# Optimization experiments

Measured on AMD Instinct MI355X. Metric: run time of the kernel, lower is better.

## Reference

```python
import jax, jax.numpy as jnp
import numpy as np
import math

B, L, DIM, H = 2, 2048, 512, 8


def setup_inputs() -> dict:
    key = jax.random.key(0)
    ks = jax.random.split(key, 8)
    s = 0.02
    return {
        "x": jax.random.normal(ks[0], (B, L, DIM), dtype=jnp.float32),
        "Wq": jax.random.normal(ks[1], (DIM, DIM), dtype=jnp.float32) * s,
        "Wk": jax.random.normal(ks[2], (DIM, DIM), dtype=jnp.float32) * s,
        "Wv": jax.random.normal(ks[3], (DIM, DIM), dtype=jnp.float32) * s,
        "Wb": jax.random.normal(ks[4], (H, DIM), dtype=jnp.float32) * s,   # content_bias weight
        "mixing": jax.random.normal(ks[5], (H, DIM), dtype=jnp.float32) * 0.2,  # UNIFORM init, std=0.2
        "Wd": jax.random.normal(ks[6], (DIM, DIM), dtype=jnp.float32) * s,
        "bd": jax.random.normal(ks[7], (DIM,), dtype=jnp.float32) * s,
    }


def reference(x, Wq, Wk, Wv, Wb, mixing, Wd, bd):
    b, l, d = x.shape
    h = mixing.shape[0]
    dh = d // h
    q = x @ Wq.T                      # [B,L,D]
    k = x @ Wk.T                      # [B,S,D]
    v = (x @ Wv.T).reshape(b, l, h, dh).transpose(0, 2, 1, 3)  # [B,H,S,dh]
    # scores[b,h,l,s] = sum_d q[b,l,d] * mixing[h,d] * k[b,s,d]
    scores = jnp.einsum("bld,hd,bsd->bhls", q, mixing, k)
    # content bias: [B,S,H] -> broadcast over query positions as [B,H,1,S]
    cb = jnp.einsum("bsd,hd->bhs", x, Wb)
    scale = math.sqrt(d / h)  # attention_head_size = dim / num_heads
    scores = (scores + cb[:, :, None, :]) / scale
    probs = jax.nn.softmax(scores, axis=-1)   # dropout disabled (eval)
    ctx = jnp.einsum("bhls,bhsd->bhld", probs, v)  # [B,H,L,dh]
    ctx = ctx.transpose(0, 2, 1, 3).reshape(b, l, d)
    return ctx @ Wd.T + bd
```

## Files before the change

### kernel.cpp

```cpp
#include <hip/hip_runtime.h>

#define B_ 2
#define L_ 2048
#define D_ 512
#define H_ 8
#define S_ 2048

typedef __attribute__((ext_vector_type(8))) short short8;
typedef __attribute__((ext_vector_type(8))) unsigned short ushort8;
typedef __attribute__((ext_vector_type(4))) unsigned short ushort4v;
typedef __attribute__((ext_vector_type(4))) float f32x4;
typedef __attribute__((ext_vector_type(16))) float f32x16;
typedef __attribute__((ext_vector_type(4))) float float4v;

__device__ __forceinline__ unsigned short f2bf(float f) {
    unsigned u = __float_as_uint(f);
    u += 0x7FFF + ((u >> 16) & 1);
    return (unsigned short)(u >> 16);
}
__device__ __forceinline__ float bf2f(unsigned short s) {
    return __uint_as_float(((unsigned)s) << 16);
}
__device__ __forceinline__ int swap23(int x) {
    return (x & ~12) | ((x & 4) << 1) | ((x & 8) >> 1);
}
__device__ __forceinline__ void async16(void* lds, const void* g) {
    __builtin_amdgcn_global_load_lds(
        (const __attribute__((address_space(1))) void*)(g),
        (__attribute__((address_space(3))) void*)(lds), 16, 0, 0);
}

__global__ __launch_bounds__(256) void cvt_cb(const float* __restrict__ x,
                                              const float* __restrict__ w0, const float* __restrict__ w1,
                                              const float* __restrict__ w2, const float* __restrict__ w3,
                                              const float* __restrict__ Wb,
                                              unsigned short* __restrict__ xb,
                                              unsigned short* __restrict__ d0, unsigned short* __restrict__ d1,
                                              unsigned short* __restrict__ d2, unsigned short* __restrict__ d3,
                                              float* __restrict__ cb) {
    if (blockIdx.x < 3072) {
        int i = blockIdx.x * 256 + threadIdx.x;
        const float* s;
        unsigned short* d;
        int idx;
        if (i < 524288) { s = x; d = xb; idx = i; }
        else {
            int off = i - 524288;
            int wsel = off >> 16; idx = off & 65535;
            s = (wsel == 0) ? w0 : (wsel == 1) ? w1 : (wsel == 2) ? w2 : w3;
            d = (wsel == 0) ? d0 : (wsel == 1) ? d1 : (wsel == 2) ? d2 : d3;
        }
        float4v v = *(const float4v*)(s + (size_t)idx * 4);
        ushort4v o;
        o[0] = f2bf(v[0]); o[1] = f2bf(v[1]); o[2] = f2bf(v[2]); o[3] = f2bf(v[3]);
        *(ushort4v*)(d + (size_t)idx * 4) = o;
    } else {
        const int tid = threadIdx.x, w = tid >> 6, lane = tid & 63;
        const int row = (blockIdx.x - 3072) * 4 + w;
        const int h = lane >> 3, seg = lane & 7;
        const float* xp = x + (size_t)row * 512 + seg * 64;
        const float* wp = Wb + (size_t)h * 512 + seg * 64;
        float acc = 0.f;
        #pragma unroll
        for (int j = 0; j < 16; ++j) {
            float4v xv = *(const float4v*)(xp + j * 4);
            float4v wv = *(const float4v*)(wp + j * 4);
            acc += xv[0] * wv[0] + xv[1] * wv[1] + xv[2] * wv[2] + xv[3] * wv[3];
        }
        acc += __shfl_xor(acc, 1);
        acc += __shfl_xor(acc, 2);
        acc += __shfl_xor(acc, 4);
        if (seg == 0) {
            int b = row >> 11, s = row & 2047;
            cb[((size_t)(b * H_ + h)) * S_ + s] = acc * 0.125f;
        }
    }
}

__device__ __forceinline__ void gemm128_core(const unsigned short* __restrict__ Ap,
                                             const unsigned short* __restrict__ Bp,
                                             short* sA, short* sB, int tid, f32x4 c[4][4]) {
    const int w = tid >> 6, lane = tid & 63, quad = lane >> 4, l15 = lane & 15;
    const int wm = (w >> 1) * 64, wn = (w & 1) * 64;
    for (int kc = 0; kc < 8; ++kc) {
        __syncthreads();
        #pragma unroll
        for (int j = 0; j < 4; ++j) {
            int i = tid + j * 256;
            int row = i >> 3, seg = i & 7;
            *(ushort8*)&sA[row * 72 + seg * 8] = *(const ushort8*)(Ap + (size_t)row * 512 + kc * 64 + seg * 8);
            *(ushort8*)&sB[row * 72 + seg * 8] = *(const ushort8*)(Bp + (size_t)row * 512 + kc * 64 + seg * 8);
        }
        __syncthreads();
        #pragma unroll
        for (int ks = 0; ks < 2; ++ks) {
            short8 a[4], b[4];
            #pragma unroll
            for (int ii = 0; ii < 4; ++ii)
                a[ii] = *(const short8*)&sA[(wm + ii * 16 + l15) * 72 + ks * 32 + quad * 8];
            #pragma unroll
            for (int jj = 0; jj < 4; ++jj)
                b[jj] = *(const short8*)&sB[(wn + jj * 16 + l15) * 72 + ks * 32 + quad * 8];
            #pragma unroll
            for (int ii = 0; ii < 4; ++ii)
                #pragma unroll
                for (int jj = 0; jj < 4; ++jj)
                    c[ii][jj] = __builtin_amdgcn_mfma_f32_16x16x32_bf16(a[ii], b[jj], c[ii][jj], 0, 0, 0);
        }
    }
}

__global__ __launch_bounds__(256) void gemm_qkv(const unsigned short* __restrict__ xb,
                                                const unsigned short* __restrict__ Wqb,
                                                const unsigned short* __restrict__ Wkb,
                                                const unsigned short* __restrict__ Wvb,
                                                unsigned short* __restrict__ qb,
                                                unsigned short* __restrict__ kpack,
                                                unsigned short* __restrict__ vfrag) {
    __shared__ short sA[128 * 72];
    __shared__ short sB[128 * 72];
    const int m0 = blockIdx.x * 128, n0 = blockIdx.y * 128, z = blockIdx.z;
    const unsigned short* Bsel = (z == 0) ? Wqb : ((z == 1) ? Wkb : Wvb);
    f32x4 c[4][4];
    #pragma unroll
    for (int ii = 0; ii < 4; ++ii)
        #pragma unroll
        for (int jj = 0; jj < 4; ++jj) { f32x4 zv = {0.f, 0.f, 0.f, 0.f}; c[ii][jj] = zv; }
    gemm128_core(xb + (size_t)m0 * 512, Bsel + (size_t)n0 * 512, sA, sB, threadIdx.x, c);
    const int tid = threadIdx.x, w = tid >> 6, lane = tid & 63, quad = lane >> 4, l15 = lane & 15;
    const int wm = (w >> 1) * 64, wn = (w & 1) * 64;
    #pragma unroll
    for (int ii = 0; ii < 4; ++ii) {
        const int mb = m0 + wm + ii * 16 + quad * 4;
        const int bb = mb >> 11;
        if (z == 0) {
            #pragma unroll
            for (int jj = 0; jj < 4; ++jj) {
                int ncol = n0 + wn + jj * 16 + l15;
                #pragma unroll
                for (int r = 0; r < 4; ++r)
                    qb[(size_t)(mb + r) * 512 + ncol] = f2bf(c[ii][jj][r]);
            }
        } else if (z == 1) {
            #pragma unroll
            for (int jj = 0; jj < 4; ++jj) {
                int d = n0 + wn + jj * 16 + l15;
                int f = d >> 4, hid = (d >> 3) & 1, jq = d & 7;
                #pragma unroll
                for (int r = 0; r < 4; ++r) {
                    int s = (mb + r) & 2047;
                    int t = s >> 5, rr = swap23(s & 31);
                    kpack[(((size_t)(bb * 64 + t)) * 32 + f) * 512 + hid * 256 + rr * 8 + jq]
                        = f2bf(c[ii][jj][r]);
                }
            }
        } else {
            const int hh = (n0 + wn) >> 6;
            const int s = mb & 2047;
            #pragma unroll
            for (int jj = 0; jj < 4; ++jj) {
                int dh = jj * 16 + l15;
                ushort4v o;
                o[0] = f2bf(c[ii][jj][0]); o[1] = f2bf(c[ii][jj][1]);
                o[2] = f2bf(c[ii][jj][2]); o[3] = f2bf(c[ii][jj][3]);
                size_t blk = ((size_t)(bb * H_ + hh) * 64 + (s >> 5)) * 4
                           + ((dh >> 5) * 2 + ((s >> 4) & 1));
                *(ushort4v*)(vfrag + blk * 512 + (dh & 31) * 8 + ((s >> 3) & 1) * 256 + (s & 7)) = o;
            }
        }
    }
}

__global__ __launch_bounds__(256) void gemm_out(const unsigned short* __restrict__ ctxb,
                                                const unsigned short* __restrict__ Wdb,
                                                const float* __restrict__ bd,
                                                float* __restrict__ out) {
    __shared__ short sA[128 * 72];
    __shared__ short sB[128 * 72];
    const int m0 = blockIdx.x * 128, n0 = blockIdx.y * 128;
    f32x4 c[4][4];
    #pragma unroll
    for (int ii = 0; ii < 4; ++ii)
        #pragma unroll
        for (int jj = 0; jj < 4; ++jj) { f32x4 zv = {0.f, 0.f, 0.f, 0.f}; c[ii][jj] = zv; }
    gemm128_core(ctxb + (size_t)m0 * 512, Wdb + (size_t)n0 * 512, sA, sB, threadIdx.x, c);
    const int tid = threadIdx.x, w = tid >> 6, lane = tid & 63, quad = lane >> 4, l15 = lane & 15;
    const int wm = (w >> 1) * 64, wn = (w & 1) * 64;
    #pragma unroll
    for (int ii = 0; ii < 4; ++ii) {
        const int mb = m0 + wm + ii * 16 + quad * 4;
        #pragma unroll
        for (int jj = 0; jj < 4; ++jj) {
            int ncol = n0 + wn + jj * 16 + l15;
            float bias = bd[ncol];
            #pragma unroll
            for (int r = 0; r < 4; ++r)
                out[(size_t)(mb + r) * 512 + ncol] = c[ii][jj][r] + bias;
        }
    }
}

__global__ __launch_bounds__(256, 2) void flash_attn(const unsigned short* __restrict__ qb,
                                                     const unsigned short* __restrict__ kpack,
                                                     const unsigned short* __restrict__ vfrag,
                                                     const float* __restrict__ cb_all,
                                                     const float* __restrict__ mixing,
                                                     _Float16* __restrict__ Opart,
                                                     float* __restrict__ lpart) {
    __shared__ short sK[4][8192];
    const int bid = blockIdx.x;
    const int half = bid & 1, b = (bid >> 1) & 1, h = (bid >> 2) & 7, qt = bid >> 5;
    const int tid = threadIdx.x, w = tid >> 6, lane = tid & 63;
    const int l31 = lane & 31, hi = lane >> 5;
    const int q0 = qt * 128 + w * 32;
    const unsigned short* kbase = kpack + ((size_t)(b * 64 + half * 32)) * 32 * 512;
    const unsigned short* vfb = vfrag + ((size_t)(b * H_ + h) * 64 + half * 32) * 2048;
    const float* cbp = cb_all + (size_t)(b * H_ + h) * S_ + half * 1024;
    const float* mixh = mixing + h * D_;

    short8 qf[32];
    {
        const unsigned short* qrow = qb + ((size_t)(b * L_) + q0 + l31) * D_ + hi * 8;
        #pragma unroll
        for (int i = 0; i < 32; ++i) {
            ushort8 qv = *(const ushort8*)(qrow + i * 16);
            float4v ma = *(const float4v*)(mixh + i * 16 + hi * 8);
            float4v mb = *(const float4v*)(mixh + i * 16 + hi * 8 + 4);
            short8 ov;
            ov[0] = (short)f2bf(bf2f(qv[0]) * ma[0]);
            ov[1] = (short)f2bf(bf2f(qv[1]) * ma[1]);
            ov[2] = (short)f2bf(bf2f(qv[2]) * ma[2]);
            ov[3] = (short)f2bf(bf2f(qv[3]) * ma[3]);
            ov[4] = (short)f2bf(bf2f(qv[4]) * mb[0]);
            ov[5] = (short)f2bf(bf2f(qv[5]) * mb[1]);
            ov[6] = (short)f2bf(bf2f(qv[6]) * mb[2]);
            ov[7] = (short)f2bf(bf2f(qv[7]) * mb[3]);
            qf[i] = ov;
        }
    }
    asm volatile("s_waitcnt vmcnt(0)" ::: "memory");

    f32x16 acco0, acco1;
    #pragma unroll
    for (int i = 0; i < 16; ++i) { acco0[i] = 0.f; acco1[i] = 0.f; }
    float lsum = 0.f;
    f32x16 accsA, accsB;
    short8 av00, av01, av10, av11;

    auto stageK = [&](int p) {
        const char* src = (const char*)(kbase + (size_t)p * 8192);
        char* dst = (char*)&sK[p & 3][0];
        #pragma unroll
        for (int ii = 0; ii < 4; ++ii)
            async16(dst + w * 1024 + ii * 4096, src + w * 1024 + ii * 4096 + (size_t)lane * 16);
    };
    auto ldV = [&](int t) {
        const unsigned short* vp = vfb + (size_t)t * 2048 + lane * 8;
        av00 = *(const short8*)(vp);
        av01 = *(const short8*)(vp + 512);
        av10 = *(const short8*)(vp + 1024);
        av11 = *(const short8*)(vp + 1536);
        asm volatile("" ::: "memory");
    };
    auto qk_chunk = [&](const short* buf, int qbase) {
        __builtin_amdgcn_s_setprio(1);
        #pragma unroll
        for (int f = 0; f < 16; ++f) {
            short8 a = *(const short8*)&buf[f * 512 + lane * 8];
            if (f & 1) accsB = __builtin_amdgcn_mfma_f32_32x32x16_bf16(a, qf[qbase + f], accsB, 0, 0, 0);
            else       accsA = __builtin_amdgcn_mfma_f32_32x32x16_bf16(a, qf[qbase + f], accsA, 0, 0, 0);
        }
        __builtin_amdgcn_s_setprio(0);
    };
    auto softmax_pv = [&](int t) {
        const int s0 = t * 32;
        float p[16];
        #pragma unroll
        for (int R = 0; R < 16; ++R) {
            const int cr = (R & 3) + 8 * (R >> 2);
            const int idx = s0 + cr - 4 * ((R >> 2) & 1);
            float cbA = cbp[idx];
            float cbB = cbp[idx + 8];
            float cbv = hi ? cbB : cbA;
            float pe = __expf((accsA[R] + accsB[R]) * 0.125f + cbv);
            p[R] = pe;
            lsum += pe;
        }
        union { unsigned int u[4]; short8 s8; } P0, P1;
        #pragma unroll
        for (int j = 0; j < 4; ++j) {
            P0.u[j] = __builtin_amdgcn_perm(__float_as_uint(p[2 * j + 1]) + 0x8000u,
                                            __float_as_uint(p[2 * j]) + 0x8000u, 0x07060302u);
            P1.u[j] = __builtin_amdgcn_perm(__float_as_uint(p[8 + 2 * j + 1]) + 0x8000u,
                                            __float_as_uint(p[8 + 2 * j]) + 0x8000u, 0x07060302u);
        }
        __builtin_amdgcn_s_setprio(1);
        acco0 = __builtin_amdgcn_mfma_f32_32x32x16_bf16(av00, P0.s8, acco0, 0, 0, 0);
        acco0 = __builtin_amdgcn_mfma_f32_32x32x16_bf16(av01, P1.s8, acco0, 0, 0, 0);
        acco1 = __builtin_amdgcn_mfma_f32_32x32x16_bf16(av10, P0.s8, acco1, 0, 0, 0);
        acco1 = __builtin_amdgcn_mfma_f32_32x32x16_bf16(av11, P1.s8, acco1, 0, 0, 0);
        __builtin_amdgcn_s_setprio(0);
    };

    stageK(0); stageK(1); stageK(2);

    for (int t = 0; t < 31; ++t) {
        #pragma unroll
        for (int i = 0; i < 16; ++i) { accsA[i] = 0.f; accsB[i] = 0.f; }
        const short* be = &sK[(t & 1) << 1][0];
        const short* bo = &sK[((t & 1) << 1) | 1][0];
        asm volatile("s_waitcnt vmcnt(8)" ::: "memory");
        __builtin_amdgcn_s_barrier();
        ldV(t);
        stageK(2 * t + 3);
        qk_chunk(be, 0);
        asm volatile("s_waitcnt vmcnt(12)" ::: "memory");
        __builtin_amdgcn_s_barrier();
        if (t < 30) stageK(2 * t + 4);
        qk_chunk(bo, 16);
        asm volatile("s_waitcnt vmcnt(8)" ::: "memory");
        softmax_pv(t);
    }
    {
        #pragma unroll
        for (int i = 0; i < 16; ++i) { accsA[i] = 0.f; accsB[i] = 0.f; }
        asm volatile("s_waitcnt vmcnt(8)" ::: "memory");
        __builtin_amdgcn_s_barrier();
        ldV(31);
        qk_chunk(&sK[2][0], 0);
        asm volatile("s_waitcnt vmcnt(4)" ::: "memory");
        __builtin_amdgcn_s_barrier();
        qk_chunk(&sK[3][0], 16);
        asm volatile("s_waitcnt vmcnt(0)" ::: "memory");
        softmax_pv(31);
    }

    lsum += __shfl_xor(lsum, 32);
    if (hi == 0) lpart[(size_t)bid * 128 + w * 32 + l31] = lsum;
    #pragma unroll
    for (int R = 0; R < 16; ++R) {
        int dh = (R & 3) + 8 * (R >> 2) + 4 * hi;
        Opart[((size_t)bid * 64 + dh) * 128 + w * 32 + l31] = (_Float16)acco0[R];
        Opart[((size_t)bid * 64 + 32 + dh) * 128 + w * 32 + l31] = (_Float16)acco1[R];
    }
}

__global__ __launch_bounds__(256) void merge_ctx(const _Float16* __restrict__ Opart,
                                                 const float* __restrict__ lpart,
                                                 unsigned short* __restrict__ ctxb) {
    int t = blockIdx.x * 256 + threadIdx.x;
    int qq = t & 127, dh4 = (t >> 7) & 15, qt = (t >> 11) & 15, h = (t >> 15) & 7, b = t >> 18;
    int base = (qt << 5) | (h << 2) | (b << 1);
    float l = lpart[(size_t)base * 128 + qq] + lpart[(size_t)(base + 1) * 128 + qq];
    float inv = 1.f / l;
    ushort4v o;
    #pragma unroll
    for (int e = 0; e < 4; ++e) {
        int dh = dh4 * 4 + e;
        float v = (float)Opart[((size_t)base * 64 + dh) * 128 + qq]
                + (float)Opart[((size_t)(base + 1) * 64 + dh) * 128 + qq];
        o[e] = f2bf(v * inv);
    }
    *(ushort4v*)(ctxb + ((size_t)(b * L_) + qt * 128 + qq) * 512 + h * 64 + dh4 * 4) = o;
}

extern "C" void kernel_launch(void* const* d_in, const int* in_sizes, int n_in,
                              void* d_out, int out_size, void* d_ws, size_t ws_size,
                              hipStream_t stream) {
    (void)in_sizes; (void)n_in; (void)out_size; (void)ws_size;
    const float* x      = (const float*)d_in[0];
    const float* Wq     = (const float*)d_in[1];
    const float* Wk     = (const float*)d_in[2];
    const float* Wv     = (const float*)d_in[3];
    const float* Wb     = (const float*)d_in[4];
    const float* mixing = (const float*)d_in[5];
    const float* Wd     = (const float*)d_in[6];
    const float* bd     = (const float*)d_in[7];
    float* out = (float*)d_out;

    char* ws = (char*)d_ws;
    const size_t MiB = 1048576;
    unsigned short* xb    = (unsigned short*)(ws);
    unsigned short* qb    = (unsigned short*)(ws + 4 * MiB);
    unsigned short* kpack = (unsigned short*)(ws + 8 * MiB);
    unsigned short* vfrag = (unsigned short*)(ws + 12 * MiB);
    unsigned short* ctxb  = (unsigned short*)(ws + 16 * MiB);
    unsigned short* Wqb   = (unsigned short*)(ws + 20 * MiB);
    unsigned short* Wkb   = (unsigned short*)(ws + 20 * MiB + 512 * 1024);
    unsigned short* Wvb   = (unsigned short*)(ws + 21 * MiB);
    unsigned short* Wdb   = (unsigned short*)(ws + 21 * MiB + 512 * 1024);
    float* cbuf           = (float*)(ws + 22 * MiB);
    float* lpart          = (float*)(ws + 23 * MiB);
    _Float16* Opart       = (_Float16*)(ws + 24 * MiB);

    cvt_cb<<<4096, 256, 0, stream>>>(x, Wq, Wk, Wv, Wd, Wb, xb, Wqb, Wkb, Wvb, Wdb, cbuf);
    gemm_qkv<<<dim3(32, 4, 3), 256, 0, stream>>>(xb, Wqb, Wkb, Wvb, qb, kpack, vfrag);
    flash_attn<<<512, 256, 0, stream>>>(qb, kpack, vfrag, cbuf, mixing, Opart, lpart);
    merge_ctx<<<2048, 256, 0, stream>>>(Opart, lpart, ctxb);
    gemm_out<<<dim3(32, 4), 256, 0, stream>>>(ctxb, Wdb, bd, out);
}
```

Baseline: 217.6 us.

## Switch QK score MFMAs to FP8 with scaled K/Q and bf16 content bias

Measured after the change: 200.6 us. -7.8%, faster.

```diff
diff --git a/kernel.cpp b/kernel.cpp
--- a/kernel.cpp
+++ b/kernel.cpp
@@ -20,6 +20,18 @@
 }
 __device__ __forceinline__ float bf2f(unsigned short s) {
     return __uint_as_float(((unsigned)s) << 16);
+}
+__device__ __forceinline__ unsigned char f2fp8(float f) {
+    return (unsigned char)(__builtin_amdgcn_cvt_pk_fp8_f32(f, f, 0, false) & 0xff);
+}
+__device__ __forceinline__ long pack8fp8(const float* v) {
+    int lo = __builtin_amdgcn_cvt_pk_fp8_f32(v[0], v[1], 0, false);
+    lo = __builtin_amdgcn_cvt_pk_fp8_f32(v[2], v[3], lo, true);
+    int hi = __builtin_amdgcn_cvt_pk_fp8_f32(v[4], v[5], 0, false);
+    hi = __builtin_amdgcn_cvt_pk_fp8_f32(v[6], v[7], hi, true);
+    union { int i[2]; long l; } u;
+    u.i[0] = lo; u.i[1] = hi;
+    return u.l;
 }
 __device__ __forceinline__ int swap23(int x) {
     return (x & ~12) | ((x & 4) << 1) | ((x & 8) >> 1);
@@ -37,7 +49,7 @@
                                               unsigned short* __restrict__ xb,
                                               unsigned short* __restrict__ d0, unsigned short* __restrict__ d1,
                                               unsigned short* __restrict__ d2, unsigned short* __restrict__ d3,
-                                              float* __restrict__ cb) {
+                                              unsigned short* __restrict__ cb) {
     if (blockIdx.x < 3072) {
         int i = blockIdx.x * 256 + threadIdx.x;
         const float* s;
@@ -72,7 +84,7 @@
         acc += __shfl_xor(acc, 4);
         if (seg == 0) {
             int b = row >> 11, s = row & 2047;
-            cb[((size_t)(b * H_ + h)) * S_ + s] = acc * 0.125f;
+            cb[((size_t)(b * H_ + h)) * S_ + s] = f2bf(acc * 0.125f);
         }
     }
 }
@@ -115,7 +127,7 @@
                                                 const unsigned short* __restrict__ Wkb,
                                                 const unsigned short* __restrict__ Wvb,
                                                 unsigned short* __restrict__ qb,
-                                                unsigned short* __restrict__ kpack,
+                                                unsigned char* __restrict__ kpack8,
                                                 unsigned short* __restrict__ vfrag) {
     __shared__ short sA[128 * 72];
     __shared__ short sB[128 * 72];
@@ -145,13 +157,13 @@
             #pragma unroll
             for (int jj = 0; jj < 4; ++jj) {
                 int d = n0 + wn + jj * 16 + l15;
-                int f = d >> 4, hid = (d >> 3) & 1, jq = d & 7;
+                int pair = d >> 5, fh = (d >> 4) & 1, hid = (d >> 3) & 1, jq = d & 7;
                 #pragma unroll
                 for (int r = 0; r < 4; ++r) {
                     int s = (mb + r) & 2047;
                     int t = s >> 5, rr = swap23(s & 31);
-                    kpack[(((size_t)(bb * 64 + t)) * 32 + f) * 512 + hid * 256 + rr * 8 + jq]
-                        = f2bf(c[ii][jj][r]);
+                    kpack8[(((size_t)(bb * 64 + t) * 16 + pair) << 10)
+                           + (hid * 32 + rr) * 16 + fh * 8 + jq] = f2fp8(c[ii][jj][r] * 32.f);
                 }
             }
         } else {
@@ -201,24 +213,24 @@
 }
 
 __global__ __launch_bounds__(256, 2) void flash_attn(const unsigned short* __restrict__ qb,
-                                                     const unsigned short* __restrict__ kpack,
+                                                     const unsigned char* __restrict__ kpack8,
                                                      const unsigned short* __restrict__ vfrag,
-                                                     const float* __restrict__ cb_all,
+                                                     const unsigned short* __restrict__ cb_all,
                                                      const float* __restrict__ mixing,
                                                      _Float16* __restrict__ Opart,
                                                      float* __restrict__ lpart) {
-    __shared__ short sK[4][8192];
+    __shared__ char sK[4][8192];
     const int bid = blockIdx.x;
     const int half = bid & 1, b = (bid >> 1) & 1, h = (bid >> 2) & 7, qt = bid >> 5;
     const int tid = threadIdx.x, w = tid >> 6, lane = tid & 63;
     const int l31 = lane & 31, hi = lane >> 5;
     const int q0 = qt * 128 + w * 32;
-    const unsigned short* kbase = kpack + ((size_t)(b * 64 + half * 32)) * 32 * 512;
+    const unsigned char* kbase = kpack8 + (((size_t)(b * 64 + half * 32)) << 14);
     const unsigned short* vfb = vfrag + ((size_t)(b * H_ + h) * 64 + half * 32) * 2048;
-    const float* cbp = cb_all + (size_t)(b * H_ + h) * S_ + half * 1024;
+    const unsigned short* cbq = cb_all + (size_t)(b * H_ + h) * S_ + half * 1024;
     const float* mixh = mixing + h * D_;
 
-    short8 qf[32];
+    long qq[32];
     {
         const unsigned short* qrow = qb + ((size_t)(b * L_) + q0 + l31) * D_ + hi * 8;
         #pragma unroll
@@ -226,16 +238,16 @@
             ushort8 qv = *(const ushort8*)(qrow + i * 16);
             float4v ma = *(const float4v*)(mixh + i * 16 + hi * 8);
             float4v mb = *(const float4v*)(mixh + i * 16 + hi * 8 + 4);
-            short8 ov;
-            ov[0] = (short)f2bf(bf2f(qv[0]) * ma[0]);
-            ov[1] = (short)f2bf(bf2f(qv[1]) * ma[1]);
-            ov[2] = (short)f2bf(bf2f(qv[2]) * ma[2]);
-            ov[3] = (short)f2bf(bf2f(qv[3]) * ma[3]);
-            ov[4] = (short)f2bf(bf2f(qv[4]) * mb[0]);
-            ov[5] = (short)f2bf(bf2f(qv[5]) * mb[1]);
-            ov[6] = (short)f2bf(bf2f(qv[6]) * mb[2]);
-            ov[7] = (short)f2bf(bf2f(qv[7]) * mb[3]);
-            qf[i] = ov;
+            float v[8];
+            v[0] = bf2f(qv[0]) * ma[0] * 16.f;
+            v[1] = bf2f(qv[1]) * ma[1] * 16.f;
+            v[2] = bf2f(qv[2]) * ma[2] * 16.f;
+            v[3] = bf2f(qv[3]) * ma[3] * 16.f;
+            v[4] = bf2f(qv[4]) * mb[0] * 16.f;
+            v[5] = bf2f(qv[5]) * mb[1] * 16.f;
+            v[6] = bf2f(qv[6]) * mb[2] * 16.f;
+            v[7] = bf2f(qv[7]) * mb[3] * 16.f;
+            qq[i] = pack8fp8(v);
         }
     }
     asm volatile("s_waitcnt vmcnt(0)" ::: "memory");
@@ -246,12 +258,13 @@
     float lsum = 0.f;
     f32x16 accsA, accsB;
     short8 av00, av01, av10, av11;
+    ushort8 cbr0, cbr1, cbr2, cbr3;
 
     auto stageK = [&](int p) {
-        const char* src = (const char*)(kbase + (size_t)p * 8192);
-        char* dst = (char*)&sK[p & 3][0];
-        #pragma unroll
-        for (int ii = 0; ii < 4; ++ii)
+        const char* src = (const char*)kpack8 + (((size_t)(b * 64 + half * 32)) << 14) + (size_t)p * 8192;
+        char* dst = &sK[p & 3][0];
+        #pragma unroll
+        for (int ii = 0; ii < 2; ++ii)
             async16(dst + w * 1024 + ii * 4096, src + w * 1024 + ii * 4096 + (size_t)lane * 16);
     };
     auto ldV = [&](int t) {
@@ -262,27 +275,40 @@
         av11 = *(const short8*)(vp + 1536);
         asm volatile("" ::: "memory");
     };
-    auto qk_chunk = [&](const short* buf, int qbase) {
+    auto ldCB = [&](int t) {
+        const unsigned short* cp = cbq + t * 32;
+        cbr0 = *(const ushort8*)(cp);
+        cbr1 = *(const ushort8*)(cp + 8);
+        cbr2 = *(const ushort8*)(cp + 16);
+        cbr3 = *(const ushort8*)(cp + 24);
+        asm volatile("" ::: "memory");
+    };
+    auto qk_chunk = [&](const char* buf, int qbase) {
         __builtin_amdgcn_s_setprio(1);
         #pragma unroll
-        for (int f = 0; f < 16; ++f) {
-            short8 a = *(const short8*)&buf[f * 512 + lane * 8];
-            if (f & 1) accsB = __builtin_amdgcn_mfma_f32_32x32x16_bf16(a, qf[qbase + f], accsB, 0, 0, 0);
-            else       accsA = __builtin_amdgcn_mfma_f32_32x32x16_bf16(a, qf[qbase + f], accsA, 0, 0, 0);
+        for (int p = 0; p < 8; ++p) {
+            long a0, a1;
+            {
+                const long* ap = (const long*)&buf[p * 1024 + lane * 16];
+                a0 = ap[0];
+                a1 = ap[1];
+            }
+            accsA = __builtin_amdgcn_mfma_f32_32x32x16_fp8_fp8(a0, qq[qbase + 2 * p], accsA, 0, 0, 0);
+            accsB = __builtin_amdgcn_mfma_f32_32x32x16_fp8_fp8(a1, qq[qbase + 2 * p + 1], accsB, 0, 0, 0);
         }
         __builtin_amdgcn_s_setprio(0);
     };
-    auto softmax_pv = [&](int t) {
-        const int s0 = t * 32;
+    auto softmax_pv = [&]() {
         float p[16];
         #pragma unroll
         for (int R = 0; R < 16; ++R) {
             const int cr = (R & 3) + 8 * (R >> 2);
-            const int idx = s0 + cr - 4 * ((R >> 2) & 1);
-            float cbA = cbp[idx];
-            float cbB = cbp[idx + 8];
-            float cbv = hi ? cbB : cbA;
-            float pe = __expf((accsA[R] + accsB[R]) * 0.125f + cbv);
+            const int il = cr - 4 * ((R >> 2) & 1);
+            const int ih = il + 8;
+            unsigned short ca = (il < 8)  ? cbr0[il & 7] : cbr2[il & 7];
+            unsigned short cbb = (ih < 16) ? cbr1[ih & 7] : cbr3[ih & 7];
+            float cbv = bf2f(hi ? cbb : ca);
+            float pe = __expf((accsA[R] + accsB[R]) * (1.0f / 4096.0f) + cbv);
             p[R] = pe;
             lsum += pe;
         }
@@ -307,32 +333,32 @@
     for (int t = 0; t < 31; ++t) {
         #pragma unroll
         for (int i = 0; i < 16; ++i) { accsA[i] = 0.f; accsB[i] = 0.f; }
-        const short* be = &sK[(t & 1) << 1][0];
-        const short* bo = &sK[((t & 1) << 1) | 1][0];
-        asm volatile("s_waitcnt vmcnt(8)" ::: "memory");
+        const char* be = &sK[(t & 1) << 1][0];
+        const char* bo = &sK[((t & 1) << 1) | 1][0];
+        asm volatile("s_waitcnt vmcnt(4)" ::: "memory");
         __builtin_amdgcn_s_barrier();
         ldV(t);
+        ldCB(t);
         stageK(2 * t + 3);
         qk_chunk(be, 0);
         asm volatile("s_waitcnt vmcnt(12)" ::: "memory");
         __builtin_amdgcn_s_barrier();
         if (t < 30) stageK(2 * t + 4);
         qk_chunk(bo, 16);
-        asm volatile("s_waitcnt vmcnt(8)" ::: "memory");
-        softmax_pv(t);
+        softmax_pv();
     }
     {
         #pragma unroll
         for (int i = 0; i < 16; ++i) { accsA[i] = 0.f; accsB[i] = 0.f; }
+        asm volatile("s_waitcnt vmcnt(4)" ::: "memory");
+        __builtin_amdgcn_s_barrier();
+        ldV(31);
+        ldCB(31);
+        qk_chunk(&sK[2][0], 0);
         asm volatile("s_waitcnt vmcnt(8)" ::: "memory");
         __builtin_amdgcn_s_barrier();
-        ldV(31);
-        qk_chunk(&sK[2][0], 0);
-        asm volatile("s_waitcnt vmcnt(4)" ::: "memory");
-        __builtin_amdgcn_s_barrier();
         qk_chunk(&sK[3][0], 16);
-        asm volatile("s_waitcnt vmcnt(0)" ::: "memory");
-        softmax_pv(31);
+        softmax_pv();
     }
 
     lsum += __shfl_xor(lsum, 32);
@@ -380,22 +406,22 @@
 
     char* ws = (char*)d_ws;
     const size_t MiB = 1048576;
-    unsigned short* xb    = (unsigned short*)(ws);
-    unsigned short* qb    = (unsigned short*)(ws + 4 * MiB);
-    unsigned short* kpack = (unsigned short*)(ws + 8 * MiB);
-    unsigned short* vfrag = (unsigned short*)(ws + 12 * MiB);
-    unsigned short* ctxb  = (unsigned short*)(ws + 16 * MiB);
-    unsigned short* Wqb   = (unsigned short*)(ws + 20 * MiB);
-    unsigned short* Wkb   = (unsigned short*)(ws + 20 * MiB + 512 * 1024);
-    unsigned short* Wvb   = (unsigned short*)(ws + 21 * MiB);
-    unsigned short* Wdb   = (unsigned short*)(ws + 21 * MiB + 512 * 1024);
-    float* cbuf           = (float*)(ws + 22 * MiB);
-    float* lpart          = (float*)(ws + 23 * MiB);
-    _Float16* Opart       = (_Float16*)(ws + 24 * MiB);
+    unsigned short* xb     = (unsigned short*)(ws);
+    unsigned short* qb     = (unsigned short*)(ws + 4 * MiB);
+    unsigned char*  kpack8 = (unsigned char*)(ws + 8 * MiB);
+    unsigned short* vfrag  = (unsigned short*)(ws + 10 * MiB);
+    unsigned short* ctxb   = (unsigned short*)(ws + 14 * MiB);
+    unsigned short* Wqb    = (unsigned short*)(ws + 18 * MiB);
+    unsigned short* Wkb    = (unsigned short*)(ws + 18 * MiB + 512 * 1024);
+    unsigned short* Wvb    = (unsigned short*)(ws + 19 * MiB);
+    unsigned short* Wdb    = (unsigned short*)(ws + 19 * MiB + 512 * 1024);
+    unsigned short* cbuf   = (unsigned short*)(ws + 20 * MiB);
+    float* lpart           = (float*)(ws + 20 * MiB + 256 * 1024);
+    _Float16* Opart        = (_Float16*)(ws + 21 * MiB);
 
     cvt_cb<<<4096, 256, 0, stream>>>(x, Wq, Wk, Wv, Wd, Wb, xb, Wqb, Wkb, Wvb, Wdb, cbuf);
-    gemm_qkv<<<dim3(32, 4, 3), 256, 0, stream>>>(xb, Wqb, Wkb, Wvb, qb, kpack, vfrag);
-    flash_attn<<<512, 256, 0, stream>>>(qb, kpack, vfrag, cbuf, mixing, Opart, lpart);
+    gemm_qkv<<<dim3(32, 4, 3), 256, 0, stream>>>(xb, Wqb, Wkb, Wvb, qb, kpack8, vfrag);
+    flash_attn<<<512, 256, 0, stream>>>(qb, kpack8, vfrag, cbuf, mixing, Opart, lpart);
     merge_ctx<<<2048, 256, 0, stream>>>(Opart, lpart, ctxb);
     gemm_out<<<dim3(32, 4), 256, 0, stream>>>(ctxb, Wdb, bd, out);
 }
```
